# Kernel optimization log

Hardware: AMD Instinct MI355X
Metric: run time of the kernel (lower is better)

## Reference

```python
import jax, jax.numpy as jnp
import numpy as np

B, G, D = 2, 2048, 128
H, K, V = 8, 16, 16


def setup_inputs() -> dict:
    key = jax.random.key(0)
    k1, k2, k3, k4 = jax.random.split(key, 4)
    return {
        "h": jax.random.normal(k1, (B, G, D), dtype=jnp.float32),
        "W_Q": jax.random.normal(k2, (H, D, K), dtype=jnp.float32) / np.sqrt(D),
        "W_K": jax.random.normal(k3, (H, D, K), dtype=jnp.float32) / np.sqrt(D),
        "W_V": jax.random.normal(k4, (H, D, V), dtype=jnp.float32) / np.sqrt(D),
    }


def reference(h, W_Q, W_K, W_V):
    # h: [B, G, D]; per-head projections -> [B, H, G, K/V]
    compat_factor = 1.0 / np.sqrt(W_Q.shape[-1]).astype(np.float32)
    q = jnp.einsum("bgd,hdk->bhgk", h, W_Q)
    k = jnp.einsum("bgd,hdk->bhgk", h, W_K)
    v = jnp.einsum("bgd,hdv->bhgv", h, W_V)
    # compatibility: [B, H, G, G]
    compat = compat_factor * jnp.einsum("bhqk,bhmk->bhqm", q, k)
    attention = jax.nn.softmax(compat, axis=-1)
    # h_p: [B, H, G, V]
    h_p = jnp.einsum("bhqm,bhmv->bhqv", attention, v)
    return h_p
```

## Files before the change

kernel.cpp:

```cpp
#include <hip/hip_runtime.h>
#include <hip/hip_bf16.h>

constexpr int Gc = 2048, Dc = 128, Hc = 8, Kc = 16;
constexpr int NCT = 24;
constexpr int NCH = 128;
constexpr int SPLIT = 8;
constexpr int QPW = 2;
constexpr int CPS = NCH / SPLIT;

typedef __attribute__((ext_vector_type(8))) short bf16x8;
typedef __attribute__((ext_vector_type(8))) unsigned short u16x8;
typedef __attribute__((ext_vector_type(4))) float f32x4;

static __device__ __forceinline__ unsigned short f2bf(float f) {
  unsigned int u = __float_as_uint(f);
  u += 0x7FFFu + ((u >> 16) & 1u);
  return (unsigned short)(u >> 16);
}
static __device__ __forceinline__ float bf2f(unsigned short s) {
  return __uint_as_float(((unsigned int)s) << 16);
}
static __device__ __forceinline__ float fexp2(float x) {
#if __has_builtin(__builtin_amdgcn_exp2f)
  return __builtin_amdgcn_exp2f(x);
#else
  return exp2f(x);
#endif
}
static __device__ __forceinline__ unsigned int pk_bf16(float a, float b) {
  unsigned int r;
  asm("v_cvt_pk_bf16_f32 %0, %1, %2" : "=v"(r) : "v"(a), "v"(b));
  return r;
}

__global__ __launch_bounds__(256) void proj_gemm_kernel(
    const float* __restrict__ h, const float* __restrict__ Wq,
    const float* __restrict__ Wk, const float* __restrict__ Wv,
    unsigned short* __restrict__ Qhi, unsigned short* __restrict__ Qlo,
    unsigned short* __restrict__ Khi, unsigned short* __restrict__ Klo,
    unsigned short* __restrict__ Vf) {
  const int widx = blockIdx.x * 4 + (threadIdx.x >> 6);
  const int ct = widx % NCT;
  const int rt = widx / NCT;
  const int l = threadIdx.x & 63;
  const int lane15 = l & 15, g4 = l >> 4;
  const int row0 = rt * 16;
  const int mat = ct >> 3, hh = ct & 7;

  const float* W = (mat == 0 ? Wq : (mat == 1 ? Wk : Wv)) + hh * (Dc * Kc);
  const float scale = (mat == 0) ? 0.25f * 1.44269504088896f : 1.0f;
  const float* hp = h + (size_t)(row0 + lane15) * Dc + g4 * 8;

  f32x4 acc = {0.f, 0.f, 0.f, 0.f};
#pragma unroll
  for (int kc = 0; kc < 4; ++kc) {
    const float4 v0 = *(const float4*)(hp + kc * 32);
    const float4 v1 = *(const float4*)(hp + kc * 32 + 4);
    const float av[8] = {v0.x, v0.y, v0.z, v0.w, v1.x, v1.y, v1.z, v1.w};
    bf16x8 ah, al;
#pragma unroll
    for (int i = 0; i < 8; ++i) {
      const unsigned short hb = f2bf(av[i]);
      ah[i] = (short)hb;
      al[i] = (short)f2bf(av[i] - bf2f(hb));
    }
    bf16x8 bh, bl;
#pragma unroll
    for (int j = 0; j < 8; ++j) {
      const float w = W[(kc * 32 + g4 * 8 + j) * Kc + lane15] * scale;
      const unsigned short hb = f2bf(w);
      bh[j] = (short)hb;
      bl[j] = (short)f2bf(w - bf2f(hb));
    }
    acc = __builtin_amdgcn_mfma_f32_16x16x32_bf16(ah, bh, acc, 0, 0, 0);
    acc = __builtin_amdgcn_mfma_f32_16x16x32_bf16(ah, bl, acc, 0, 0, 0);
    acc = __builtin_amdgcn_mfma_f32_16x16x32_bf16(al, bh, acc, 0, 0, 0);
  }

  const int b = row0 >> 11;
  const int g0 = row0 & 2047;
  const int bhh = b * Hc + hh;
  if (mat <= 1) {
    unsigned short* dhi = (mat == 0) ? Qhi : Khi;
    unsigned short* dlo = (mat == 0) ? Qlo : Klo;
#pragma unroll
    for (int i = 0; i < 4; ++i) {
      const size_t off = ((size_t)bhh * Gc + g0 + g4 * 4 + i) * Kc + lane15;
      const unsigned short hb = f2bf(acc[i]);
      dhi[off] = hb;
      dlo[off] = f2bf(acc[i] - bf2f(hb));
    }
  } else {
    const int c = g0 >> 4;
    u16x8 fv;
#pragma unroll
    for (int i = 0; i < 4; ++i) {
      const unsigned short hb = f2bf(acc[i]);
      fv[i] = hb;
      fv[i + 4] = f2bf(acc[i] - bf2f(hb));
    }
    *(u16x8*)(Vf + ((size_t)(bhh * NCH + c) * 64 + l) * 8) = fv;
  }
}

__global__ __launch_bounds__(512) void flash_kernel(
    const unsigned short* __restrict__ Qhi, const unsigned short* __restrict__ Qlo,
    const unsigned short* __restrict__ Khi, const unsigned short* __restrict__ Klo,
    const unsigned short* __restrict__ Vf, float* __restrict__ out) {
  __shared__ f32x4 lo_s[SPLIT][QPW][64];
  __shared__ float lml[SPLIT][QPW][16][2];

  const int qg = blockIdx.x;
  const int split = threadIdx.x >> 6;
  const int bh = qg >> 6;
  const int qi0 = (qg & 63) * QPW;
  const int l = threadIdx.x & 63;
  const int lane15 = l & 15, g4 = l >> 4, dhalf = g4 & 1;

  bf16x8 bqh[QPW], bql[QPW];
#pragma unroll
  for (int t = 0; t < QPW; ++t) {
    const size_t qoff =
        ((size_t)bh * Gc + (qi0 + t) * 16 + lane15) * Kc + 8 * dhalf;
    bqh[t] = *(const bf16x8*)(Qhi + qoff);
    bql[t] = *(const bf16x8*)(Qlo + qoff);
  }

  const unsigned short* kbase = (g4 >= 2 ? Klo : Khi) +
      (size_t)bh * Gc * Kc + lane15 * Kc + 8 * dhalf;
  const unsigned short* vf = Vf + ((size_t)bh * NCH * 64 + l) * 8;

  const int c0 = split * CPS;
  const f32x4 z = {0.f, 0.f, 0.f, 0.f};
  f32x4 o[QPW] = {z, z};
  float run_max[QPW] = {-1e30f, -1e30f};
  float thr[QPW] = {-1e30f, -1e30f};
  float lsum[QPW] = {0.f, 0.f};

  for (int c = c0; c < c0 + CPS; ++c) {
    const bf16x8 ak = *(const bf16x8*)(kbase + (size_t)c * 256);
    const bf16x8 av = *(const bf16x8*)(vf + (size_t)c * 512);

#pragma unroll
    for (int t = 0; t < QPW; ++t) {
      f32x4 s = __builtin_amdgcn_mfma_f32_16x16x32_bf16(ak, bql[t], z, 0, 0, 0);
      s = __builtin_amdgcn_mfma_f32_16x16x32_bf16(ak, bqh[t], s, 0, 0, 0);

      const float cm = fmaxf(fmaxf(s[0], s[1]), fmaxf(s[2], s[3]));
      if (!__all((int)(cm <= thr[t]))) {
        float fm = fmaxf(cm, __shfl_xor(cm, 16));
        fm = fmaxf(fm, __shfl_xor(fm, 32));
        const float nm = fmaxf(run_max[t], fm);
        const float corr = fexp2(run_max[t] - nm);
        o[t][0] *= corr; o[t][1] *= corr; o[t][2] *= corr; o[t][3] *= corr;
        lsum[t] *= corr;
        run_max[t] = nm;
        thr[t] = nm + 11.5f;
      }
      const float p0 = fexp2(s[0] - run_max[t]);
      const float p1 = fexp2(s[1] - run_max[t]);
      const float p2 = fexp2(s[2] - run_max[t]);
      const float p3 = fexp2(s[3] - run_max[t]);
      lsum[t] += (p0 + p1) + (p2 + p3);

      union { bf16x8 v; unsigned int w[4]; } bp;
      const unsigned int w01 = pk_bf16(p0, p1);
      const unsigned int w23 = pk_bf16(p2, p3);
      bp.w[0] = w01; bp.w[1] = w23; bp.w[2] = w01; bp.w[3] = w23;

      o[t] = __builtin_amdgcn_mfma_f32_16x16x32_bf16(av, bp.v, o[t], 0, 0, 0);
    }
  }

#pragma unroll
  for (int t = 0; t < QPW; ++t) {
    float ls = lsum[t];
    ls += __shfl_xor(ls, 16);
    ls += __shfl_xor(ls, 32);
    lo_s[split][t][l] = o[t];
    if (l < 16) {
      lml[split][t][l][0] = run_max[t];
      lml[split][t][l][1] = ls;
    }
  }
  __syncthreads();

  if (threadIdx.x < QPW * 64) {
    const int t = split;
    float m[SPLIT], lv[SPLIT];
#pragma unroll
    for (int s = 0; s < SPLIT; ++s) {
      m[s] = lml[s][t][lane15][0];
      lv[s] = lml[s][t][lane15][1];
    }
    float M = m[0];
#pragma unroll
    for (int s = 1; s < SPLIT; ++s) M = fmaxf(M, m[s]);
    f32x4 acc = {0.f, 0.f, 0.f, 0.f};
    float den = 0.f;
#pragma unroll
    for (int s = 0; s < SPLIT; ++s) {
      const float w = fexp2(m[s] - M);
      den += w * lv[s];
      const f32x4 po = lo_s[s][t][l];
      acc[0] += w * po[0]; acc[1] += w * po[1];
      acc[2] += w * po[2]; acc[3] += w * po[3];
    }
    const float inv = 1.0f / den;
    f32x4 res;
    res[0] = acc[0] * inv; res[1] = acc[1] * inv;
    res[2] = acc[2] * inv; res[3] = acc[3] * inv;
    *(f32x4*)(out + ((size_t)bh * Gc + (qi0 + t) * 16 + lane15) * Kc + 4 * g4) =
        res;
  }
}

extern "C" void kernel_launch(void* const* d_in, const int* in_sizes, int n_in,
                              void* d_out, int out_size, void* d_ws, size_t ws_size,
                              hipStream_t stream) {
  const float* h  = (const float*)d_in[0];
  const float* Wq = (const float*)d_in[1];
  const float* Wk = (const float*)d_in[2];
  const float* Wv = (const float*)d_in[3];
  float* out = (float*)d_out;

  char* ws = (char*)d_ws;
  unsigned short* Qhi = (unsigned short*)(ws);
  unsigned short* Qlo = (unsigned short*)(ws + (1u << 20));
  unsigned short* Khi = (unsigned short*)(ws + (2u << 20));
  unsigned short* Klo = (unsigned short*)(ws + (3u << 20));
  unsigned short* Vf  = (unsigned short*)(ws + (4u << 20));

  proj_gemm_kernel<<<1536, 256, 0, stream>>>(h, Wq, Wk, Wv, Qhi, Qlo, Khi, Klo,
                                             Vf);
  flash_kernel<<<1024, 512, 0, stream>>>(Qhi, Qlo, Khi, Klo, Vf, out);
}
```

Baseline: 96.17 us.

## Share running max across query tiles and unroll flash loop for ILP

```diff
diff --git a/kernel.cpp b/kernel.cpp
--- a/kernel.cpp
+++ b/kernel.cpp
@@ -10,6 +10,7 @@
 
 typedef __attribute__((ext_vector_type(8))) short bf16x8;
 typedef __attribute__((ext_vector_type(8))) unsigned short u16x8;
+typedef __attribute__((ext_vector_type(4))) unsigned int u32x4;
 typedef __attribute__((ext_vector_type(4))) float f32x4;
 
 static __device__ __forceinline__ unsigned short f2bf(float f) {
@@ -103,7 +104,7 @@
   }
 }
 
-__global__ __launch_bounds__(512) void flash_kernel(
+__global__ __launch_bounds__(512, 6) void flash_kernel(
     const unsigned short* __restrict__ Qhi, const unsigned short* __restrict__ Qlo,
     const unsigned short* __restrict__ Khi, const unsigned short* __restrict__ Klo,
     const unsigned short* __restrict__ Vf, float* __restrict__ out) {
@@ -127,48 +128,56 @@
   }
 
   const unsigned short* kbase = (g4 >= 2 ? Klo : Khi) +
-      (size_t)bh * Gc * Kc + lane15 * Kc + 8 * dhalf;
-  const unsigned short* vf = Vf + ((size_t)bh * NCH * 64 + l) * 8;
-
-  const int c0 = split * CPS;
+      (size_t)bh * Gc * Kc + lane15 * Kc + 8 * dhalf + (size_t)split * CPS * 256;
+  const unsigned short* vbase =
+      Vf + ((size_t)bh * NCH * 64 + l) * 8 + (size_t)split * CPS * 512;
+
   const f32x4 z = {0.f, 0.f, 0.f, 0.f};
   f32x4 o[QPW] = {z, z};
-  float run_max[QPW] = {-1e30f, -1e30f};
-  float thr[QPW] = {-1e30f, -1e30f};
+  float run_max = -1e30f, thr = -1e30f;
   float lsum[QPW] = {0.f, 0.f};
 
-  for (int c = c0; c < c0 + CPS; ++c) {
+#pragma unroll 4
+  for (int c = 0; c < CPS; ++c) {
     const bf16x8 ak = *(const bf16x8*)(kbase + (size_t)c * 256);
-    const bf16x8 av = *(const bf16x8*)(vf + (size_t)c * 512);
-
+    const bf16x8 av = *(const bf16x8*)(vbase + (size_t)c * 512);
+
+    f32x4 s[QPW];
 #pragma unroll
     for (int t = 0; t < QPW; ++t) {
-      f32x4 s = __builtin_amdgcn_mfma_f32_16x16x32_bf16(ak, bql[t], z, 0, 0, 0);
-      s = __builtin_amdgcn_mfma_f32_16x16x32_bf16(ak, bqh[t], s, 0, 0, 0);
-
-      const float cm = fmaxf(fmaxf(s[0], s[1]), fmaxf(s[2], s[3]));
-      if (!__all((int)(cm <= thr[t]))) {
-        float fm = fmaxf(cm, __shfl_xor(cm, 16));
-        fm = fmaxf(fm, __shfl_xor(fm, 32));
-        const float nm = fmaxf(run_max[t], fm);
-        const float corr = fexp2(run_max[t] - nm);
+      f32x4 tmp = __builtin_amdgcn_mfma_f32_16x16x32_bf16(ak, bql[t], z, 0, 0, 0);
+      s[t] = __builtin_amdgcn_mfma_f32_16x16x32_bf16(ak, bqh[t], tmp, 0, 0, 0);
+    }
+
+    float cm = fmaxf(fmaxf(s[0][0], s[0][1]), fmaxf(s[0][2], s[0][3]));
+    cm = fmaxf(cm, fmaxf(fmaxf(s[1][0], s[1][1]), fmaxf(s[1][2], s[1][3])));
+    if (!__all((int)(cm <= thr))) {
+      float fm = fmaxf(cm, __shfl_xor(cm, 16));
+      fm = fmaxf(fm, __shfl_xor(fm, 32));
+      const float nm = fmaxf(run_max, fm);
+      const float corr = fexp2(run_max - nm);
+#pragma unroll
+      for (int t = 0; t < QPW; ++t) {
         o[t][0] *= corr; o[t][1] *= corr; o[t][2] *= corr; o[t][3] *= corr;
         lsum[t] *= corr;
-        run_max[t] = nm;
-        thr[t] = nm + 11.5f;
       }
-      const float p0 = fexp2(s[0] - run_max[t]);
-      const float p1 = fexp2(s[1] - run_max[t]);
-      const float p2 = fexp2(s[2] - run_max[t]);
-      const float p3 = fexp2(s[3] - run_max[t]);
+      run_max = nm;
+      thr = nm + 11.5f;
+    }
+
+#pragma unroll
+    for (int t = 0; t < QPW; ++t) {
+      const float p0 = fexp2(s[t][0] - run_max);
+      const float p1 = fexp2(s[t][1] - run_max);
+      const float p2 = fexp2(s[t][2] - run_max);
+      const float p3 = fexp2(s[t][3] - run_max);
       lsum[t] += (p0 + p1) + (p2 + p3);
 
-      union { bf16x8 v; unsigned int w[4]; } bp;
       const unsigned int w01 = pk_bf16(p0, p1);
       const unsigned int w23 = pk_bf16(p2, p3);
-      bp.w[0] = w01; bp.w[1] = w23; bp.w[2] = w01; bp.w[3] = w23;
-
-      o[t] = __builtin_amdgcn_mfma_f32_16x16x32_bf16(av, bp.v, o[t], 0, 0, 0);
+      const u32x4 bpv = {w01, w23, w01, w23};
+      const bf16x8 bp = __builtin_bit_cast(bf16x8, bpv);
+      o[t] = __builtin_amdgcn_mfma_f32_16x16x32_bf16(av, bp, o[t], 0, 0, 0);
     }
   }
 
@@ -179,7 +188,7 @@
     ls += __shfl_xor(ls, 32);
     lo_s[split][t][l] = o[t];
     if (l < 16) {
-      lml[split][t][l][0] = run_max[t];
+      lml[split][t][l][0] = run_max;
       lml[split][t][l][1] = ls;
     }
   }
```

Result: no change. 94.47 us (-1.8%).
